# Kernel tuning notes

Measured on AMD Instinct MI355X. Metric: run time of the kernel, lower is better.

The kernel has to match this reference:

```python
import jax, jax.numpy as jnp
import numpy as np

N = 131072
IN, HID, OUT = 128, 256, 64
NUM_TASKS = 16
NUM_COPIES = 4
NUM_LAYERS = 3


def setup_inputs() -> dict:
    key = jax.random.key(0)
    ks = jax.random.split(key, 10)
    inputs = jax.random.normal(ks[0], (N, IN), dtype=jnp.float32)
    task_indices = jax.random.randint(ks[1], (N,), 0, NUM_TASKS, dtype=jnp.int32)
    copy_maps = jax.random.randint(ks[2], (NUM_LAYERS, NUM_TASKS), 0, NUM_COPIES, dtype=jnp.int32)
    # per-copy Linear weights, Kaiming-ish scale 1/sqrt(fan_in)
    W0 = jax.random.normal(ks[3], (NUM_COPIES, IN, HID), dtype=jnp.float32) / np.sqrt(IN)
    b0 = jax.random.normal(ks[4], (NUM_COPIES, HID), dtype=jnp.float32) * 0.01
    W1 = jax.random.normal(ks[5], (NUM_COPIES, HID, HID), dtype=jnp.float32) / np.sqrt(HID)
    b1 = jax.random.normal(ks[6], (NUM_COPIES, HID), dtype=jnp.float32) * 0.01
    W2 = jax.random.normal(ks[7], (NUM_COPIES, HID, OUT), dtype=jnp.float32) / np.sqrt(HID)
    b2 = jax.random.normal(ks[8], (NUM_COPIES, OUT), dtype=jnp.float32) * 0.01
    return {"inputs": inputs, "task_indices": task_indices, "copy_maps": copy_maps,
            "W0": W0, "b0": b0, "W1": W1, "b1": b1, "W2": W2, "b2": b2}


def _routed_layer(x, W, b, copy_idx, apply_tanh):
    # x: [N, d_in], W: [C, d_in, d_out], b: [C, d_out], copy_idx: [N]
    # Each token goes through exactly one copy's Linear. Equivalent to the
    # torch sort->per-copy-forward->unsort, expressed as masked accumulation
    # over the small fixed set of copies (avoids data-dependent shapes).
    y = jnp.zeros((x.shape[0], W.shape[2]), dtype=x.dtype)
    for c in range(W.shape[0]):
        mask = (copy_idx == c).astype(x.dtype)[:, None]  # [N, 1]
        y = y + mask * (x @ W[c] + b[c])
    return jnp.tanh(y) if apply_tanh else y


def reference(inputs, task_indices, copy_maps, W0, b0, W1, b1, W2, b2):
    x = inputs
    Ws = (W0, W1, W2)
    bs = (b0, b1, b2)
    for layer in range(NUM_LAYERS):
        copy_idx = copy_maps[layer][task_indices]  # [N] task->copy routing
        x = _routed_layer(x, Ws[layer], bs[layer], copy_idx,
                          apply_tanh=(layer != NUM_LAYERS - 1))
    return x
```

## Files before the change

### kernel.cpp

```cpp
#include <hip/hip_runtime.h>

#define N_TOK 131072
#define TILE 64
#define NT_MAX 2064
#define NBLK 256

typedef __attribute__((ext_vector_type(8))) short s8v;
typedef __attribute__((ext_vector_type(4))) float f4v;
typedef unsigned short ushort_t;

__device__ __forceinline__ unsigned short f2bf(float x) {
    union { float f; unsigned u; } v; v.f = x;
    unsigned r = v.u + 0x7fffu + ((v.u >> 16) & 1u);
    return (unsigned short)(r >> 16);
}

__device__ __forceinline__ unsigned pk2(float a, float b) {
    union { float f; unsigned u; } x, y; x.f = a; y.f = b;
    return __byte_perm(x.u + 0x8000u, y.u + 0x8000u, 0x7632);
}

__device__ __forceinline__ float tanh_fast(float x) {
    float e = __builtin_amdgcn_exp2f(x * 2.8853900817779268f);
    float r = __builtin_amdgcn_rcpf(e + 1.0f);
    return __builtin_fmaf(-2.0f, r, 1.0f);
}

__global__ void prep_hist_kernel(const float* __restrict__ W0, const float* __restrict__ W1,
                                 const float* __restrict__ W2,
                                 ushort_t* __restrict__ W0p, ushort_t* __restrict__ W1p,
                                 ushort_t* __restrict__ W2p,
                                 const int* __restrict__ task, int* __restrict__ blockCounts) {
    if (blockIdx.x < 224) {
        int f = blockIdx.x * 256 + threadIdx.x;
        const float* src; ushort_t* dst; int K, N;
        if (f < 16384)      { src = W0; dst = W0p; K = 128; N = 256; }
        else if (f < 49152) { src = W1; dst = W1p; K = 256; N = 256; f -= 16384; }
        else                { src = W2; dst = W2p; K = 256; N = 64;  f -= 49152; }
        int fpc = (N >> 4) * (K >> 5) * 64;
        int c = f / fpc, r = f % fpc;
        int lane = r & 63;
        int kt = (r >> 6) % (K >> 5);
        int ftile = (r >> 6) / (K >> 5);
        int n = ftile * 16 + (lane & 15);
        int kbase = kt * 32 + (lane >> 4) * 8;
        const float* s = src + (size_t)c * K * N + (size_t)kbase * N + n;
        s8v pk;
#pragma unroll
        for (int j = 0; j < 8; j++) pk[j] = (short)f2bf(s[(size_t)j * N]);
        *reinterpret_cast<s8v*>(dst + ((size_t)(c * fpc + r) << 3)) = pk;
    } else {
        __shared__ int cnt[16];
        int t = threadIdx.x;
        int hb = blockIdx.x - 224;
        if (t < 16) cnt[t] = 0;
        __syncthreads();
        int base = hb * 2048 + t;
#pragma unroll
        for (int i = 0; i < 8; i++) atomicAdd(&cnt[task[base + i * 256]], 1);
        __syncthreads();
        if (t < 16) blockCounts[hb * 16 + t] = cnt[t];
    }
}

__global__ void sort_kernel(const int* __restrict__ task, const int* __restrict__ blockCounts,
                            int* __restrict__ tbaseG, int* __restrict__ perm) {
    __shared__ int cntLds[1024];
    __shared__ int total[16], pref[16], rank[16];
    __shared__ int tokBase[16], tbase[17];
    int t = threadIdx.x, b = blockIdx.x;
    for (int i = t; i < 1024; i += 256) cntLds[i] = blockCounts[i];
    if (t < 16) rank[t] = 0;
    __syncthreads();
    if (t < 16) {
        int tot = 0, pf = 0;
#pragma unroll
        for (int bb = 0; bb < 64; bb++) {
            int v = cntLds[bb * 16 + t];
            tot += v;
            if (bb < b) pf += v;
        }
        total[t] = tot; pref[t] = pf;
    }
    __syncthreads();
    if (t == 0) {
        int tok = 0, tile = 0;
        for (int k = 0; k < 16; k++) {
            tokBase[k] = tok;
            tbase[k] = tile;
            int ntk = (total[k] + TILE - 1) / TILE;
            tok += ntk * TILE;
            tile += ntk;
        }
        tbase[16] = tile;
    }
    __syncthreads();
    if (b == 0) {
        if (t < 17) tbaseG[t] = tbase[t];
        for (int i = t; i < 16 * TILE; i += 256) {
            int k = i >> 6, off = i & (TILE - 1);
            int idx = total[k] + off;
            int lim = ((total[k] + TILE - 1) / TILE) * TILE;
            if (idx < lim) perm[tokBase[k] + idx] = -1;
        }
    }
    int tk[8], my[8];
#pragma unroll
    for (int i = 0; i < 8; i++) {
        int idx = b * 2048 + i * 256 + t;
        tk[i] = task[idx];
        my[i] = atomicAdd(&rank[tk[i]], 1);
    }
#pragma unroll
    for (int i = 0; i < 8; i++) {
        int idx = b * 2048 + i * 256 + t;
        perm[tokBase[tk[i]] + pref[tk[i]] + my[i]] = idx;
    }
}

__launch_bounds__(512)
__attribute__((amdgpu_waves_per_eu(2, 2)))
__global__ void mlp_kernel(const float* __restrict__ x_in,
                           const int* __restrict__ cmap,
                           const float* __restrict__ b0,
                           const float* __restrict__ b1,
                           const float* __restrict__ b2,
                           const ushort_t* __restrict__ W0p,
                           const ushort_t* __restrict__ W1p,
                           const ushort_t* __restrict__ W2p,
                           const int* __restrict__ tbaseG,
                           const int* __restrict__ perm,
                           float* __restrict__ out) {
    __shared__ __align__(16) ushort_t H1[16384];
    __shared__ __align__(16) ushort_t XH2[16384];

    int p = blockIdx.x;
    int k = p >> 4, sub = p & 15;
    int tBeg = tbaseG[k], tEnd = tbaseG[k + 1];
    if (tBeg + sub >= tEnd) return;

    int t = threadIdx.x;
    int c0 = cmap[k], c1 = cmap[16 + k], c2 = cmap[32 + k];

    int w = t >> 6;
    int lane = t & 63;
    int l15 = lane & 15, lq = lane >> 4;
    int mt2 = w & 3, ntb2 = (w >> 2) * 2;

    s8v wa0[2][4], wa1[2][8], wa2r[8];
    {
        const ushort_t* Wc = W0p + (size_t)c0 * 32768;
#pragma unroll
        for (int mi = 0; mi < 2; mi++)
#pragma unroll
            for (int kt = 0; kt < 4; kt++)
                wa0[mi][kt] = *reinterpret_cast<const s8v*>(Wc + ((((2 * w + mi) * 4 + kt) * 64 + lane) << 3));
    }
    {
        const ushort_t* Wc = W1p + (size_t)c1 * 65536;
#pragma unroll
        for (int mi = 0; mi < 2; mi++)
#pragma unroll
            for (int kt = 0; kt < 8; kt++)
                wa1[mi][kt] = *reinterpret_cast<const s8v*>(Wc + ((((2 * w + mi) * 8 + kt) * 64 + lane) << 3));
    }
    {
        const ushort_t* Wc = W2p + (size_t)c2 * 16384;
#pragma unroll
        for (int kt = 0; kt < 8; kt++)
            wa2r[kt] = *reinterpret_cast<const s8v*>(Wc + (((mt2 * 8 + kt) * 64 + lane) << 3));
    }
    f4v bv0[2], bv1[2], bv2;
#pragma unroll
    for (int mi = 0; mi < 2; mi++) {
        bv0[mi] = *reinterpret_cast<const f4v*>(b0 + c0 * 256 + (2 * w + mi) * 16 + lq * 4);
        bv1[mi] = *reinterpret_cast<const f4v*>(b1 + c1 * 256 + (2 * w + mi) * 16 + lq * 4);
    }
    bv2 = *reinterpret_cast<const f4v*>(b2 + c2 * 64 + mt2 * 16 + lq * 4);

    int r = t >> 3, q = t & 7;
    const float4* xbase = reinterpret_cast<const float4*>(x_in);
    float4 v0 = make_float4(0.f, 0.f, 0.f, 0.f), v1 = v0, v2 = v0, v3 = v0;
    int ptok = -1;

    int tile = tBeg + sub;
    {
        ptok = perm[tile * TILE + r];
        if ((unsigned)ptok < (unsigned)N_TOK) {
            const float4* src = xbase + (size_t)ptok * 32 + q * 4;
            v0 = src[0]; v1 = src[1]; v2 = src[2]; v3 = src[3];
        }
    }

    for (; tile < tEnd; tile += 16) {
        {
            int fragid = (r >> 4) * 4 + (q >> 1);
            int lp0 = (r & 15) + 16 * ((q & 1) * 2);
            uint4 pk0, pk1;
            pk0.x = pk2(v0.x, v0.y); pk0.y = pk2(v0.z, v0.w);
            pk0.z = pk2(v1.x, v1.y); pk0.w = pk2(v1.z, v1.w);
            pk1.x = pk2(v2.x, v2.y); pk1.y = pk2(v2.z, v2.w);
            pk1.z = pk2(v3.x, v3.y); pk1.w = pk2(v3.z, v3.w);
            *reinterpret_cast<uint4*>(&XH2[(fragid * 64 + lp0) << 3]) = pk0;
            *reinterpret_cast<uint4*>(&XH2[(fragid * 64 + lp0 + 16) << 3]) = pk1;
        }
        int ntile = tile + 16;
        if (ntile < tEnd) {
            ptok = perm[ntile * TILE + r];
            float4 z = make_float4(0.f, 0.f, 0.f, 0.f);
            float4 a0 = z, a1 = z, a2 = z, a3 = z;
            if ((unsigned)ptok < (unsigned)N_TOK) {
                const float4* src = xbase + (size_t)ptok * 32 + q * 4;
                a0 = src[0]; a1 = src[1]; a2 = src[2]; a3 = src[3];
            }
            v0 = a0; v1 = a1; v2 = a2; v3 = a3;
        }
        __syncthreads();

        {
            f4v acc[2][4];
#pragma unroll
            for (int mi = 0; mi < 2; mi++)
#pragma unroll
                for (int nt = 0; nt < 4; nt++)
                    acc[mi][nt] = bv0[mi];
#pragma unroll
            for (int kt = 0; kt < 4; kt++) {
                s8v xb[4];
#pragma unroll
                for (int nt = 0; nt < 4; nt++)
                    xb[nt] = *reinterpret_cast<const s8v*>(&XH2[((nt * 4 + kt) * 64 + lane) << 3]);
#pragma unroll
                for (int mi = 0; mi < 2; mi++)
#pragma unroll
                    for (int nt = 0; nt < 4; nt++)
                        acc[mi][nt] = __builtin_amdgcn_mfma_f32_16x16x32_bf16(wa0[mi][kt], xb[nt], acc[mi][nt], 0, 0, 0);
            }
#pragma unroll
            for (int mi = 0; mi < 2; mi++) {
                int ft = 2 * w + mi;
                int kt_h = ft >> 1;
                int lanep = l15 + 16 * ((ft & 1) * 2 + (lq >> 1));
                int j0 = (lq & 1) * 4;
#pragma unroll
                for (int nt = 0; nt < 4; nt++) {
                    float t0 = tanh_fast(acc[mi][nt][0]);
                    float t1 = tanh_fast(acc[mi][nt][1]);
                    float t2 = tanh_fast(acc[mi][nt][2]);
                    float t3 = tanh_fast(acc[mi][nt][3]);
                    uint2 pk; pk.x = pk2(t0, t1); pk.y = pk2(t2, t3);
                    *reinterpret_cast<uint2*>(&H1[(((nt * 8 + kt_h) * 64 + lanep) << 3) + j0]) = pk;
                }
            }
        }
        __syncthreads();

        {
            f4v acc[2][4];
#pragma unroll
            for (int mi = 0; mi < 2; mi++)
#pragma unroll
                for (int nt = 0; nt < 4; nt++)
                    acc[mi][nt] = bv1[mi];
#pragma unroll
            for (int kt = 0; kt < 8; kt++) {
                s8v xb[4];
#pragma unroll
                for (int nt = 0; nt < 4; nt++)
                    xb[nt] = *reinterpret_cast<const s8v*>(&H1[((nt * 8 + kt) * 64 + lane) << 3]);
#pragma unroll
                for (int mi = 0; mi < 2; mi++)
#pragma unroll
                    for (int nt = 0; nt < 4; nt++)
                        acc[mi][nt] = __builtin_amdgcn_mfma_f32_16x16x32_bf16(wa1[mi][kt], xb[nt], acc[mi][nt], 0, 0, 0);
            }
#pragma unroll
            for (int mi = 0; mi < 2; mi++) {
                int ft = 2 * w + mi;
                int kt_h = ft >> 1;
                int lanep = l15 + 16 * ((ft & 1) * 2 + (lq >> 1));
                int j0 = (lq & 1) * 4;
#pragma unroll
                for (int nt = 0; nt < 4; nt++) {
                    float t0 = tanh_fast(acc[mi][nt][0]);
                    float t1 = tanh_fast(acc[mi][nt][1]);
                    float t2 = tanh_fast(acc[mi][nt][2]);
                    float t3 = tanh_fast(acc[mi][nt][3]);
                    uint2 pk; pk.x = pk2(t0, t1); pk.y = pk2(t2, t3);
                    *reinterpret_cast<uint2*>(&XH2[(((nt * 8 + kt_h) * 64 + lanep) << 3) + j0]) = pk;
                }
            }
        }
        __syncthreads();

        {
            int tok0 = perm[tile * TILE + ntb2 * 16 + l15];
            int tok1 = perm[tile * TILE + (ntb2 + 1) * 16 + l15];
            f4v acc[2];
#pragma unroll
            for (int e = 0; e < 2; e++)
                acc[e] = bv2;
#pragma unroll
            for (int kt = 0; kt < 8; kt++) {
#pragma unroll
                for (int e = 0; e < 2; e++) {
                    s8v xb = *reinterpret_cast<const s8v*>(&XH2[(((ntb2 + e) * 8 + kt) * 64 + lane) << 3]);
                    acc[e] = __builtin_amdgcn_mfma_f32_16x16x32_bf16(wa2r[kt], xb, acc[e], 0, 0, 0);
                }
            }
#pragma unroll
            for (int e = 0; e < 2; e++) {
                int tok = e ? tok1 : tok0;
                if ((unsigned)tok < (unsigned)N_TOK) {
                    float4 o;
                    o.x = acc[e][0]; o.y = acc[e][1]; o.z = acc[e][2]; o.w = acc[e][3];
                    *reinterpret_cast<float4*>(out + (size_t)tok * 64 + mt2 * 16 + lq * 4) = o;
                }
            }
        }
        __syncthreads();
    }
}

extern "C" void kernel_launch(void* const* d_in, const int* in_sizes, int n_in,
                              void* d_out, int out_size, void* d_ws, size_t ws_size,
                              hipStream_t stream) {
    const float* inputs = (const float*)d_in[0];
    const int*   task   = (const int*)d_in[1];
    const int*   cmap   = (const int*)d_in[2];
    const float* W0     = (const float*)d_in[3];
    const float* b0     = (const float*)d_in[4];
    const float* W1     = (const float*)d_in[5];
    const float* b1     = (const float*)d_in[6];
    const float* W2     = (const float*)d_in[7];
    const float* b2     = (const float*)d_in[8];
    float* out = (float*)d_out;

    char* ws = (char*)d_ws;
    int* blockCounts = (int*)(ws + 0);
    int* tbaseG      = (int*)(ws + 4096);
    int* perm        = (int*)(ws + 4224);
    ushort_t* W0p    = (ushort_t*)(ws + 532608);
    ushort_t* W1p    = (ushort_t*)(ws + 794752);
    ushort_t* W2p    = (ushort_t*)(ws + 1319040);

    prep_hist_kernel<<<288, 256, 0, stream>>>(W0, W1, W2, W0p, W1p, W2p, task, blockCounts);
    sort_kernel<<<64, 256, 0, stream>>>(task, blockCounts, tbaseG, perm);
    mlp_kernel<<<NBLK, 512, 0, stream>>>(inputs, cmap, b0, b1, b2,
                                         W0p, W1p, W2p, tbaseG, perm, out);
}
```

Measured before the change: 161.6 us.

## Stage half of layer-1 weights in LDS and reload rest per tile

Instead of holding all layer-1 weight fragments in registers, the first half of W1 for the block's copy is staged in LDS once, and the second half is reloaded from global memory on every tile. Block indexing is also remapped so consecutive blocks interleave across tasks. The aim is to cut register pressure, switching from an explicit waves-per-EU attribute to launch_bounds(512,2). The cost is extra LDS traffic (LDS use grows to 128KB per block), repeated global weight loads inside the tile loop, and a risk that the larger LDS footprint limits occupancy.

```diff
diff --git a/kernel.cpp b/kernel.cpp
--- a/kernel.cpp
+++ b/kernel.cpp
@@ -118,8 +118,7 @@
     }
 }
 
-__launch_bounds__(512)
-__attribute__((amdgpu_waves_per_eu(2, 2)))
+__launch_bounds__(512, 2)
 __global__ void mlp_kernel(const float* __restrict__ x_in,
                            const int* __restrict__ cmap,
                            const float* __restrict__ b0,
@@ -133,9 +132,11 @@
                            float* __restrict__ out) {
     __shared__ __align__(16) ushort_t H1[16384];
     __shared__ __align__(16) ushort_t XH2[16384];
+    __shared__ __align__(16) ushort_t W1lds[32768];
 
     int p = blockIdx.x;
-    int k = p >> 4, sub = p & 15;
+    int x = p & 7, s = p >> 3;
+    int k = 2 * x + (s >> 4), sub = s & 15;
     int tBeg = tbaseG[k], tEnd = tbaseG[k + 1];
     if (tBeg + sub >= tEnd) return;
 
@@ -147,29 +148,26 @@
     int l15 = lane & 15, lq = lane >> 4;
     int mt2 = w & 3, ntb2 = (w >> 2) * 2;
 
-    s8v wa0[2][4], wa1[2][8], wa2r[8];
-    {
-        const ushort_t* Wc = W0p + (size_t)c0 * 32768;
-#pragma unroll
-        for (int mi = 0; mi < 2; mi++)
-#pragma unroll
-            for (int kt = 0; kt < 4; kt++)
-                wa0[mi][kt] = *reinterpret_cast<const s8v*>(Wc + ((((2 * w + mi) * 4 + kt) * 64 + lane) << 3));
-    }
-    {
-        const ushort_t* Wc = W1p + (size_t)c1 * 65536;
-#pragma unroll
-        for (int mi = 0; mi < 2; mi++)
-#pragma unroll
-            for (int kt = 0; kt < 8; kt++)
-                wa1[mi][kt] = *reinterpret_cast<const s8v*>(Wc + ((((2 * w + mi) * 8 + kt) * 64 + lane) << 3));
-    }
-    {
-        const ushort_t* Wc = W2p + (size_t)c2 * 16384;
-#pragma unroll
-        for (int kt = 0; kt < 8; kt++)
-            wa2r[kt] = *reinterpret_cast<const s8v*>(Wc + (((mt2 * 8 + kt) * 64 + lane) << 3));
-    }
+    const ushort_t* Wc0 = W0p + (size_t)c0 * 32768;
+    const ushort_t* Wc1 = W1p + (size_t)c1 * 65536;
+    const ushort_t* Wc2 = W2p + (size_t)c2 * 16384;
+
+    for (int i = t; i < 4096; i += 512) {
+        int fp = i >> 6, ln = i & 63;
+        int sf = fp + ((fp >> 2) << 2);
+        *reinterpret_cast<s8v*>(&W1lds[i << 3]) =
+            *reinterpret_cast<const s8v*>(Wc1 + ((((size_t)sf << 6) + ln) << 3));
+    }
+
+    s8v wa0[2][4], wa2r[8];
+#pragma unroll
+    for (int mi = 0; mi < 2; mi++)
+#pragma unroll
+        for (int kt = 0; kt < 4; kt++)
+            wa0[mi][kt] = *reinterpret_cast<const s8v*>(Wc0 + ((((2 * w + mi) * 4 + kt) * 64 + lane) << 3));
+#pragma unroll
+    for (int kt = 0; kt < 8; kt++)
+        wa2r[kt] = *reinterpret_cast<const s8v*>(Wc2 + (((mt2 * 8 + kt) * 64 + lane) << 3));
     f4v bv0[2], bv1[2], bv2;
 #pragma unroll
     for (int mi = 0; mi < 2; mi++) {
@@ -181,7 +179,7 @@
     int r = t >> 3, q = t & 7;
     const float4* xbase = reinterpret_cast<const float4*>(x_in);
     float4 v0 = make_float4(0.f, 0.f, 0.f, 0.f), v1 = v0, v2 = v0, v3 = v0;
-    int ptok = -1;
+    int ptok;
 
     int tile = tBeg + sub;
     {
@@ -262,8 +260,18 @@
 #pragma unroll
                 for (int nt = 0; nt < 4; nt++)
                     acc[mi][nt] = bv1[mi];
-#pragma unroll
-            for (int kt = 0; kt < 8; kt++) {
+            s8v wa1b[2][4];
+#pragma unroll
+            for (int mi = 0; mi < 2; mi++)
+#pragma unroll
+                for (int kt = 0; kt < 4; kt++)
+                    wa1b[mi][kt] = *reinterpret_cast<const s8v*>(Wc1 + ((((2 * w + mi) * 8 + kt + 4) * 64 + lane) << 3));
+#pragma unroll
+            for (int kt = 0; kt < 4; kt++) {
+                s8v wa[2];
+#pragma unroll
+                for (int mi = 0; mi < 2; mi++)
+                    wa[mi] = *reinterpret_cast<const s8v*>(&W1lds[(((2 * w + mi) * 4 + kt) * 64 + lane) << 3]);
                 s8v xb[4];
 #pragma unroll
                 for (int nt = 0; nt < 4; nt++)
@@ -272,7 +280,19 @@
                 for (int mi = 0; mi < 2; mi++)
 #pragma unroll
                     for (int nt = 0; nt < 4; nt++)
-                        acc[mi][nt] = __builtin_amdgcn_mfma_f32_16x16x32_bf16(wa1[mi][kt], xb[nt], acc[mi][nt], 0, 0, 0);
+                        acc[mi][nt] = __builtin_amdgcn_mfma_f32_16x16x32_bf16(wa[mi], xb[nt], acc[mi][nt], 0, 0, 0);
+            }
+#pragma unroll
+            for (int kt = 0; kt < 4; kt++) {
+                s8v xb[4];
+#pragma unroll
+                for (int nt = 0; nt < 4; nt++)
+                    xb[nt] = *reinterpret_cast<const s8v*>(&H1[((nt * 8 + kt + 4) * 64 + lane) << 3]);
+#pragma unroll
+                for (int mi = 0; mi < 2; mi++)
+#pragma unroll
+                    for (int nt = 0; nt < 4; nt++)
+                        acc[mi][nt] = __builtin_amdgcn_mfma_f32_16x16x32_bf16(wa1b[mi][kt], xb[nt], acc[mi][nt], 0, 0, 0);
             }
 #pragma unroll
             for (int mi = 0; mi < 2; mi++) {
@@ -297,9 +317,7 @@
             int tok0 = perm[tile * TILE + ntb2 * 16 + l15];
             int tok1 = perm[tile * TILE + (ntb2 + 1) * 16 + l15];
             f4v acc[2];
-#pragma unroll
-            for (int e = 0; e < 2; e++)
-                acc[e] = bv2;
+            acc[0] = bv2; acc[1] = bv2;
 #pragma unroll
             for (int kt = 0; kt < 8; kt++) {
 #pragma unroll
```

Measured after the change: 162.8 us. About the same (+0.8%).

## Stream weights from global per k-step and double-buffer X tile in LDS

Applied to the files above, without the earlier changes.

Drops the register-resident weight fragments and instead reloads weight fragments from global/L2 inside each k-loop iteration, freeing many VGPRs. The launch bound changes to ask for two blocks per CU, and the input tile gets its own double-buffered LDS region, written during layer 2. This removes one barrier per tile and remaps blocks to tasks. The trade is repeated weight loads on every tile, which may stall the MFMA chain on load latency, against higher occupancy.

```diff
diff --git a/kernel.cpp b/kernel.cpp
--- a/kernel.cpp
+++ b/kernel.cpp
@@ -118,8 +118,7 @@
     }
 }
 
-__launch_bounds__(512)
-__attribute__((amdgpu_waves_per_eu(2, 2)))
+__launch_bounds__(512, 2)
 __global__ void mlp_kernel(const float* __restrict__ x_in,
                            const int* __restrict__ cmap,
                            const float* __restrict__ b0,
@@ -131,11 +130,13 @@
                            const int* __restrict__ tbaseG,
                            const int* __restrict__ perm,
                            float* __restrict__ out) {
+    __shared__ __align__(16) ushort_t Xb[2][8192];
     __shared__ __align__(16) ushort_t H1[16384];
-    __shared__ __align__(16) ushort_t XH2[16384];
+    __shared__ __align__(16) ushort_t H2[16384];
 
     int p = blockIdx.x;
-    int k = p >> 4, sub = p & 15;
+    int x = p & 7, s = p >> 3;
+    int k = 2 * x + (s >> 4), sub = s & 15;
     int tBeg = tbaseG[k], tEnd = tbaseG[k + 1];
     if (tBeg + sub >= tEnd) return;
 
@@ -147,29 +148,10 @@
     int l15 = lane & 15, lq = lane >> 4;
     int mt2 = w & 3, ntb2 = (w >> 2) * 2;
 
-    s8v wa0[2][4], wa1[2][8], wa2r[8];
-    {
-        const ushort_t* Wc = W0p + (size_t)c0 * 32768;
-#pragma unroll
-        for (int mi = 0; mi < 2; mi++)
-#pragma unroll
-            for (int kt = 0; kt < 4; kt++)
-                wa0[mi][kt] = *reinterpret_cast<const s8v*>(Wc + ((((2 * w + mi) * 4 + kt) * 64 + lane) << 3));
-    }
-    {
-        const ushort_t* Wc = W1p + (size_t)c1 * 65536;
-#pragma unroll
-        for (int mi = 0; mi < 2; mi++)
-#pragma unroll
-            for (int kt = 0; kt < 8; kt++)
-                wa1[mi][kt] = *reinterpret_cast<const s8v*>(Wc + ((((2 * w + mi) * 8 + kt) * 64 + lane) << 3));
-    }
-    {
-        const ushort_t* Wc = W2p + (size_t)c2 * 16384;
-#pragma unroll
-        for (int kt = 0; kt < 8; kt++)
-            wa2r[kt] = *reinterpret_cast<const s8v*>(Wc + (((mt2 * 8 + kt) * 64 + lane) << 3));
-    }
+    const ushort_t* Wc0 = W0p + (size_t)c0 * 32768;
+    const ushort_t* Wc1 = W1p + (size_t)c1 * 65536;
+    const ushort_t* Wc2 = W2p + (size_t)c2 * 16384;
+
     f4v bv0[2], bv1[2], bv2;
 #pragma unroll
     for (int mi = 0; mi < 2; mi++) {
@@ -179,43 +161,41 @@
     bv2 = *reinterpret_cast<const f4v*>(b2 + c2 * 64 + mt2 * 16 + lq * 4);
 
     int r = t >> 3, q = t & 7;
+    int fragid = (r >> 4) * 4 + (q >> 1);
+    int lp0 = (r & 15) + 16 * ((q & 1) * 2);
     const float4* xbase = reinterpret_cast<const float4*>(x_in);
-    float4 v0 = make_float4(0.f, 0.f, 0.f, 0.f), v1 = v0, v2 = v0, v3 = v0;
-    int ptok = -1;
 
     int tile = tBeg + sub;
     {
-        ptok = perm[tile * TILE + r];
+        int ptok = perm[tile * TILE + r];
+        float4 v0 = make_float4(0.f, 0.f, 0.f, 0.f), v1 = v0, v2 = v0, v3 = v0;
         if ((unsigned)ptok < (unsigned)N_TOK) {
             const float4* src = xbase + (size_t)ptok * 32 + q * 4;
             v0 = src[0]; v1 = src[1]; v2 = src[2]; v3 = src[3];
         }
-    }
-
+        uint4 pk0, pk1;
+        pk0.x = pk2(v0.x, v0.y); pk0.y = pk2(v0.z, v0.w);
+        pk0.z = pk2(v1.x, v1.y); pk0.w = pk2(v1.z, v1.w);
+        pk1.x = pk2(v2.x, v2.y); pk1.y = pk2(v2.z, v2.w);
+        pk1.z = pk2(v3.x, v3.y); pk1.w = pk2(v3.z, v3.w);
+        *reinterpret_cast<uint4*>(&Xb[0][(fragid * 64 + lp0) << 3]) = pk0;
+        *reinterpret_cast<uint4*>(&Xb[0][(fragid * 64 + lp0 + 16) << 3]) = pk1;
+    }
+    __syncthreads();
+
+    int cur = 0;
     for (; tile < tEnd; tile += 16) {
-        {
-            int fragid = (r >> 4) * 4 + (q >> 1);
-            int lp0 = (r & 15) + 16 * ((q & 1) * 2);
-            uint4 pk0, pk1;
-            pk0.x = pk2(v0.x, v0.y); pk0.y = pk2(v0.z, v0.w);
-            pk0.z = pk2(v1.x, v1.y); pk0.w = pk2(v1.z, v1.w);
-            pk1.x = pk2(v2.x, v2.y); pk1.y = pk2(v2.z, v2.w);
-            pk1.z = pk2(v3.x, v3.y); pk1.w = pk2(v3.z, v3.w);
-            *reinterpret_cast<uint4*>(&XH2[(fragid * 64 + lp0) << 3]) = pk0;
-            *reinterpret_cast<uint4*>(&XH2[(fragid * 64 + lp0 + 16) << 3]) = pk1;
-        }
         int ntile = tile + 16;
-        if (ntile < tEnd) {
-            ptok = perm[ntile * TILE + r];
-            float4 z = make_float4(0.f, 0.f, 0.f, 0.f);
-            float4 a0 = z, a1 = z, a2 = z, a3 = z;
+        bool hasNext = ntile < tEnd;
+
+        float4 a0 = make_float4(0.f, 0.f, 0.f, 0.f), a1 = a0, a2 = a0, a3 = a0;
+        if (hasNext) {
+            int ptok = perm[ntile * TILE + r];
             if ((unsigned)ptok < (unsigned)N_TOK) {
                 const float4* src = xbase + (size_t)ptok * 32 + q * 4;
                 a0 = src[0]; a1 = src[1]; a2 = src[2]; a3 = src[3];
             }
-            v0 = a0; v1 = a1; v2 = a2; v3 = a3;
-        }
-        __syncthreads();
+        }
 
         {
             f4v acc[2][4];
@@ -226,15 +206,18 @@
                     acc[mi][nt] = bv0[mi];
 #pragma unroll
             for (int kt = 0; kt < 4; kt++) {
-                s8v xb[4];
+                s8v wa[2], xb[4];
+#pragma unroll
+                for (int mi = 0; mi < 2; mi++)
+                    wa[mi] = *reinterpret_cast<const s8v*>(Wc0 + ((((2 * w + mi) * 4 + kt) * 64 + lane) << 3));
 #pragma unroll
                 for (int nt = 0; nt < 4; nt++)
-                    xb[nt] = *reinterpret_cast<const s8v*>(&XH2[((nt * 4 + kt) * 64 + lane) << 3]);
+                    xb[nt] = *reinterpret_cast<const s8v*>(&Xb[cur][((nt * 4 + kt) * 64 + lane) << 3]);
 #pragma unroll
                 for (int mi = 0; mi < 2; mi++)
 #pragma unroll
                     for (int nt = 0; nt < 4; nt++)
-                        acc[mi][nt] = __builtin_amdgcn_mfma_f32_16x16x32_bf16(wa0[mi][kt], xb[nt], acc[mi][nt], 0, 0, 0);
+                        acc[mi][nt] = __builtin_amdgcn_mfma_f32_16x16x32_bf16(wa[mi], xb[nt], acc[mi][nt], 0, 0, 0);
             }
 #pragma unroll
             for (int mi = 0; mi < 2; mi++) {
@@ -264,7 +247,10 @@
                     acc[mi][nt] = bv1[mi];
 #pragma unroll
             for (int kt = 0; kt < 8; kt++) {
-                s8v xb[4];
+                s8v wa[2], xb[4];
+#pragma unroll
+                for (int mi = 0; mi < 2; mi++)
+                    wa[mi] = *reinterpret_cast<const s8v*>(Wc1 + ((((2 * w + mi) * 8 + kt) * 64 + lane) << 3));
 #pragma unroll
                 for (int nt = 0; nt < 4; nt++)
                     xb[nt] = *reinterpret_cast<const s8v*>(&H1[((nt * 8 + kt) * 64 + lane) << 3]);
@@ -272,7 +258,16 @@
                 for (int mi = 0; mi < 2; mi++)
 #pragma unroll
                     for (int nt = 0; nt < 4; nt++)
-                        acc[mi][nt] = __builtin_amdgcn_mfma_f32_16x16x32_bf16(wa1[mi][kt], xb[nt], acc[mi][nt], 0, 0, 0);
+                        acc[mi][nt] = __builtin_amdgcn_mfma_f32_16x16x32_bf16(wa[mi], xb[nt], acc[mi][nt], 0, 0, 0);
+            }
+            if (hasNext) {
+                uint4 pk0, pk1;
+                pk0.x = pk2(a0.x, a0.y); pk0.y = pk2(a0.z, a0.w);
+                pk0.z = pk2(a1.x, a1.y); pk0.w = pk2(a1.z, a1.w);
+                pk1.x = pk2(a2.x, a2.y); pk1.y = pk2(a2.z, a2.w);
+                pk1.z = pk2(a3.x, a3.y); pk1.w = pk2(a3.z, a3.w);
+                *reinterpret_cast<uint4*>(&Xb[cur ^ 1][(fragid * 64 + lp0) << 3]) = pk0;
+                *reinterpret_cast<uint4*>(&Xb[cur ^ 1][(fragid * 64 + lp0 + 16) << 3]) = pk1;
             }
 #pragma unroll
             for (int mi = 0; mi < 2; mi++) {
@@ -287,7 +282,7 @@
                     float t2 = tanh_fast(acc[mi][nt][2]);
                     float t3 = tanh_fast(acc[mi][nt][3]);
                     uint2 pk; pk.x = pk2(t0, t1); pk.y = pk2(t2, t3);
-                    *reinterpret_cast<uint2*>(&XH2[(((nt * 8 + kt_h) * 64 + lanep) << 3) + j0]) = pk;
+                    *reinterpret_cast<uint2*>(&H2[(((nt * 8 + kt_h) * 64 + lanep) << 3) + j0]) = pk;
                 }
             }
         }
@@ -297,15 +292,14 @@
             int tok0 = perm[tile * TILE + ntb2 * 16 + l15];
             int tok1 = perm[tile * TILE + (ntb2 + 1) * 16 + l15];
             f4v acc[2];
-#pragma unroll
-            for (int e = 0; e < 2; e++)
-                acc[e] = bv2;
+            acc[0] = bv2; acc[1] = bv2;
 #pragma unroll
             for (int kt = 0; kt < 8; kt++) {
+                s8v wa = *reinterpret_cast<const s8v*>(Wc2 + (((mt2 * 8 + kt) * 64 + lane) << 3));
 #pragma unroll
                 for (int e = 0; e < 2; e++) {
-                    s8v xb = *reinterpret_cast<const s8v*>(&XH2[(((ntb2 + e) * 8 + kt) * 64 + lane) << 3]);
-                    acc[e] = __builtin_amdgcn_mfma_f32_16x16x32_bf16(wa2r[kt], xb, acc[e], 0, 0, 0);
+                    s8v xb = *reinterpret_cast<const s8v*>(&H2[(((ntb2 + e) * 8 + kt) * 64 + lane) << 3]);
+                    acc[e] = __builtin_amdgcn_mfma_f32_16x16x32_bf16(wa, xb, acc[e], 0, 0, 0);
                 }
             }
 #pragma unroll
@@ -319,6 +313,7 @@
             }
         }
         __syncthreads();
+        cur ^= 1;
     }
 }
 
```

Result: no change. 162.5 us (+0.6%).
